# Optimization experiments

Measured on AMD Instinct MI355X. Metric: run time of the kernel, lower is better.

Reference implementation:

```python
import jax, jax.numpy as jnp
import numpy as np

B, N, D, H = 16, 576, 1024, 16
HD = D // H


def make_rel_indices(num_patches):
    # ConViT rel_indices: [N, N, 3] = (dx, dy, dx^2+dy^2) on a sqrt(N) grid
    img = int(num_patches ** 0.5)
    coords = np.arange(img)
    ind = coords.reshape(1, -1) - coords.reshape(-1, 1)  # [img, img]
    indx = np.tile(ind, (img, img))                      # repeats within rows
    indy = np.repeat(np.repeat(ind, img, axis=0), img, axis=1)
    indd = indx ** 2 + indy ** 2
    rel = np.stack([indx, indy, indd], axis=-1).astype(np.float32)  # [N, N, 3]
    return jnp.asarray(rel)


def setup_inputs() -> dict:
    key = jax.random.key(0)
    ks = jax.random.split(key, 8)
    s = D ** -0.5
    return {
        "x": jax.random.normal(ks[0], (B, N, D), jnp.float32),
        "W_qk": jax.random.normal(ks[1], (D, 2 * D), jnp.float32) * s,
        "W_v": jax.random.normal(ks[2], (D, D), jnp.float32) * s,
        "W_proj": jax.random.normal(ks[3], (D, D), jnp.float32) * s,
        "b_proj": jnp.zeros((D,), jnp.float32),
        "W_pos": jax.random.normal(ks[4], (3, H), jnp.float32) * 0.5,
        "b_pos": jnp.zeros((H,), jnp.float32),
        "gating": jnp.ones((H,), jnp.float32),
        "rel_indices": make_rel_indices(N),
    }


def reference(x, W_qk, W_v, W_proj, b_proj, W_pos, b_pos, gating, rel_indices):
    scale = HD ** -0.5
    qk = x @ W_qk                                  # [B, N, 2D]
    q = qk[..., :D].reshape(B, N, H, HD).transpose(0, 2, 1, 3)  # [B,H,N,HD]
    k = qk[..., D:].reshape(B, N, H, HD).transpose(0, 2, 1, 3)
    # content attention
    patch_score = jax.nn.softmax(jnp.einsum('bhnd,bhmd->bhnm', q, k) * scale, axis=-1)
    # learned positional attention from relative coordinates
    pos_logits = rel_indices @ W_pos + b_pos       # [N, N, H]
    pos_score = jax.nn.softmax(jnp.transpose(pos_logits, (2, 0, 1))[None], axis=-1)  # [1,H,N,N]
    # per-head gating mix, renormalized
    g = jax.nn.sigmoid(gating)[None, :, None, None]
    attn = (1.0 - g) * patch_score + g * pos_score
    attn = attn / attn.sum(axis=-1, keepdims=True)
    v = (x @ W_v).reshape(B, N, H, HD).transpose(0, 2, 1, 3)    # [B,H,N,HD]
    out = jnp.einsum('bhnm,bhmd->bhnd', attn, v)
    out = out.transpose(0, 2, 1, 3).reshape(B, N, D)
    return out @ W_proj + b_proj
```

## Files before the change

kernel.cpp:

```cpp
#include <hip/hip_runtime.h>
#include <hip/hip_bf16.h>
#include <math.h>

#define B_ 16
#define N_ 576
#define D_ 1024
#define H_ 16
#define HD_ 64
#define BN_ (B_ * N_)
#define LOG2E 1.4426950408889634f

typedef __bf16 bf16x8 __attribute__((ext_vector_type(8)));
typedef __bf16 bf16x4 __attribute__((ext_vector_type(4)));
typedef float  f32x4  __attribute__((ext_vector_type(4)));
typedef unsigned int u32x4 __attribute__((ext_vector_type(4)));

__device__ __forceinline__ unsigned pack_bf16x2(float a, float b)
{
    __bf16 lo = (__bf16)a, hi = (__bf16)b;
    unsigned short ul = __builtin_bit_cast(unsigned short, lo);
    unsigned short uh = __builtin_bit_cast(unsigned short, hi);
    return (unsigned)ul | ((unsigned)uh << 16);
}

__global__ __launch_bounds__(256) void prep(
    const float* __restrict__ x, const float* __restrict__ W_qk,
    const float* __restrict__ W_v, const float* __restrict__ W_proj,
    const float* __restrict__ W_pos, const float* __restrict__ gating,
    __bf16* __restrict__ xb, __bf16* __restrict__ wqkvt,
    __bf16* __restrict__ wpt, __bf16* __restrict__ Pp)
{
    __shared__ float t[64][65];
    const int bid = blockIdx.x;
    const int tid = threadIdx.x;

    if (bid < 9216) {
        size_t i = ((size_t)bid * 256 + tid) * 4;
        float4 v = *(const float4*)&x[i];
        bf16x4 o;
        o.x = (__bf16)v.x; o.y = (__bf16)v.y; o.z = (__bf16)v.z; o.w = (__bf16)v.w;
        *(bf16x4*)&xb[i] = o;
    } else if (bid < 10240) {
        int idx = bid - 9216;
        const float* W; __bf16* Wt; int N, bx, by;
        if (idx < 512)      { W = W_qk;   Wt = wqkvt;                          N = 2 * D_; bx = idx & 31; by = idx >> 5; }
        else if (idx < 768) { idx -= 512; W = W_v;    Wt = wqkvt + (size_t)2 * D_ * D_; N = D_; bx = idx & 15; by = idx >> 4; }
        else                { idx -= 768; W = W_proj; Wt = wpt;                N = D_;     bx = idx & 15; by = idx >> 4; }
        const int k0 = by * 64, n0 = bx * 64;
        const int r = tid >> 4, c4 = (tid & 15) << 2;
#pragma unroll
        for (int s = 0; s < 4; ++s) {
            int rr = r + (s << 4);
            float4 w = *(const float4*)&W[(size_t)(k0 + rr) * N + n0 + c4];
            t[rr][c4] = w.x; t[rr][c4 + 1] = w.y; t[rr][c4 + 2] = w.z; t[rr][c4 + 3] = w.w;
        }
        __syncthreads();
#pragma unroll
        for (int s = 0; s < 4; ++s) {
            int rr = r + (s << 4);
            bf16x4 o;
            o.x = (__bf16)t[c4 + 0][rr]; o.y = (__bf16)t[c4 + 1][rr];
            o.z = (__bf16)t[c4 + 2][rr]; o.w = (__bf16)t[c4 + 3][rr];
            *(bf16x4*)&Wt[(size_t)(n0 + rr) * D_ + k0 + c4] = o;
        }
    } else {
        int flat = (bid - 10240) * 4 + (tid >> 6);
        int h = flat / N_, n = flat % N_;
        int lane = tid & 63;
        const float w0 = W_pos[h] * LOG2E, w1 = W_pos[H_ + h] * LOG2E,
                    w2 = W_pos[2 * H_ + h] * LOG2E;
        const float rx = (float)(n % 24), ry = (float)(n / 24);
        float l2[9];
        float mx = -1e30f;
#pragma unroll
        for (int i = 0; i < 9; ++i) {
            int m = lane + (i << 6);
            float cx = (float)(m % 24), cy = (float)(m / 24);
            float dx = cx - rx, dy = cy - ry;
            float l = fmaf(w2, fmaf(dx, dx, dy * dy), fmaf(w0, dx, w1 * dy));
            l2[i] = l;
            mx = fmaxf(mx, l);
        }
#pragma unroll
        for (int off = 32; off; off >>= 1) mx = fmaxf(mx, __shfl_xor(mx, off, 64));
        float sum = 0.f;
#pragma unroll
        for (int i = 0; i < 9; ++i) sum += __builtin_amdgcn_exp2f(l2[i] - mx);
#pragma unroll
        for (int off = 32; off; off >>= 1) sum += __shfl_xor(sum, off, 64);
        float g = 1.f / (1.f + __expf(-gating[h]));
        float c = __log2f(g) - mx - __log2f(sum);
        __bf16* row = Pp + (size_t)(h * N_ + n) * N_;
#pragma unroll
        for (int i = 0; i < 9; ++i)
            row[(i << 6) + lane] = (__bf16)__builtin_amdgcn_exp2f(l2[i] + c);
    }
}

template<int OUTMODE>
__global__ __launch_bounds__(512, 2) void gemm256(
    const __bf16* __restrict__ A, const __bf16* __restrict__ Bt,
    const float* __restrict__ bias, void* __restrict__ Cp, void* __restrict__ Cp2,
    int M, int N, int nbn)
{
    __shared__ __bf16 As[2][256 * 64];
    __shared__ __bf16 Bs[2][256 * 64];

    const int tid = threadIdx.x;
    const int lane = tid & 63, wave = tid >> 6;
    const int fr = lane & 15, quad = lane >> 4;

    const int nwg = gridDim.x;
    const int wg = ((int)blockIdx.x & 7) * (nwg >> 3) + ((int)blockIdx.x >> 3);
    const int m0 = (wg / nbn) * 256;
    const int n0 = (wg % nbn) * 256;

    const int wm = (wave >> 2) * 128;
    const int wn = (wave & 3) * 64;

    int offA[2], offB[2], dA[2], dB[2];
#pragma unroll
    for (int r = 0; r < 2; ++r) {
        int rl = r * 64 + (tid >> 3);
        int pc = tid & 7;
        int l  = pc ^ (rl & 7);
        int rowA = (rl & 63) | ((rl & 64) << 1);
        int rowB = (rl & 31) + ((rl >> 5) << 6);
        offA[r] = (m0 + rowA) * 1024 + l * 8;
        offB[r] = (n0 + rowB) * 1024 + l * 8;
        int rlb = r * 64 + wave * 8;
        int rowAb = (rlb & 63) | ((rlb & 64) << 1);
        int rowBb = (rlb & 31) + ((rlb >> 5) << 6);
        dA[r] = rowAb * 64;
        dB[r] = rowBb * 64;
    }

    const int cA0 = (quad ^ (fr & 7)) * 8;
    const int cA1 = ((4 + quad) ^ (fr & 7)) * 8;

    f32x4 acc[8][4];
#pragma unroll
    for (int i = 0; i < 8; ++i)
#pragma unroll
        for (int j = 0; j < 4; ++j)
            acc[i][j] = (f32x4){0.f, 0.f, 0.f, 0.f};

    bf16x8 af[2][4];
    bf16x8 bfr[2][2][2];

#define GLL16(src, dst) __builtin_amdgcn_global_load_lds( \
    (const __attribute__((address_space(1))) void*)(src), \
    (__attribute__((address_space(3))) void*)(dst), 16, 0, 0)

#define ISSUE_A(U, BUF, KOFF) { \
    GLL16(A + offA[0] + (U) * 65536 + (KOFF), &As[BUF][dA[0] + (U) * 4096]); \
    GLL16(A + offA[1] + (U) * 65536 + (KOFF), &As[BUF][dA[1] + (U) * 4096]); }
#define ISSUE_B(U, BUF, KOFF) { \
    GLL16(Bt + offB[0] + (U) * 32768 + (KOFF), &Bs[BUF][dB[0] + (U) * 2048]); \
    GLL16(Bt + offB[1] + (U) * 32768 + (KOFF), &Bs[BUF][dB[1] + (U) * 2048]); }

#define READ_A(BUF, MH) { \
    const __bf16* _p = &As[BUF][(wm + (MH) * 64 + fr) * 64]; \
    _Pragma("unroll") for (int i = 0; i < 4; ++i) { \
        af[0][i] = *(const bf16x8*)&_p[i * 1024 + cA0]; \
        af[1][i] = *(const bf16x8*)&_p[i * 1024 + cA1]; } }

#define READ_B(BUF, NH) { \
    const __bf16* _p = &Bs[BUF][(wn + (NH) * 32 + fr) * 64]; \
    _Pragma("unroll") for (int j = 0; j < 2; ++j) { \
        bfr[NH][0][j] = *(const bf16x8*)&_p[j * 1024 + cA0]; \
        bfr[NH][1][j] = *(const bf16x8*)&_p[j * 1024 + cA1]; } }

#define MFMAQ(MH, NH) { \
    __builtin_amdgcn_s_setprio(1); \
    _Pragma("unroll") for (int i = 0; i < 4; ++i) \
    _Pragma("unroll") for (int j = 0; j < 2; ++j) { \
        f32x4 c = acc[(MH) * 4 + i][(NH) * 2 + j]; \
        c = __builtin_amdgcn_mfma_f32_16x16x32_bf16(af[0][i], bfr[NH][0][j], c, 0, 0, 0); \
        c = __builtin_amdgcn_mfma_f32_16x16x32_bf16(af[1][i], bfr[NH][1][j], c, 0, 0, 0); \
        acc[(MH) * 4 + i][(NH) * 2 + j] = c; } \
    __builtin_amdgcn_s_setprio(0); }

#define WAITV(N) asm volatile("s_waitcnt vmcnt(" #N ")" ::: "memory")
#define BARL() { asm volatile("s_waitcnt lgkmcnt(0)" ::: "memory"); \
                 asm volatile("s_barrier" ::: "memory"); }

#define ITER4(LAST) { \
   ISSUE_A(0, 1, kodd); ISSUE_B(0, 1, kodd); WAITV(6); BARL(); \
        READ_A(0, 0); READ_B(0, 0); READ_B(0, 1); MFMAQ(0, 0); MFMAQ(0, 1); \
   ISSUE_B(1, 1, kodd); ISSUE_A(1, 1, kodd); WAITV(8); BARL(); \
        READ_A(0, 1); MFMAQ(1, 0); MFMAQ(1, 1); \
   if (!(LAST)) { ISSUE_A(0, 0, keven); ISSUE_B(0, 0, keven); WAITV(6); } \
                       else { WAITV(2); } BARL(); \
        READ_A(1, 0); READ_B(1, 0); READ_B(1, 1); MFMAQ(0, 0); MFMAQ(0, 1); \
   if (!(LAST)) { ISSUE_B(1, 0, keven); ISSUE_A(1, 0, keven); WAITV(8); } \
                       else { WAITV(0); } BARL(); \
        READ_A(1, 1); MFMAQ(1, 0); MFMAQ(1, 1); }

    ISSUE_A(0, 0, 0); ISSUE_B(0, 0, 0); ISSUE_B(1, 0, 0); ISSUE_A(1, 0, 0);

#pragma unroll 1
    for (int it = 0; it < 7; ++it) {
        const int kodd  = it * 128 + 64;
        const int keven = it * 128 + 128;
        ITER4(0);
    }
    {
        const int kodd  = 7 * 128 + 64;
        const int keven = 0;
        ITER4(1);
    }

#undef ITER4
#undef WAITV
#undef BARL
#undef MFMAQ
#undef READ_B
#undef READ_A
#undef ISSUE_B
#undef ISSUE_A
#undef GLL16

    const int colb = n0 + wn + fr;
    const int rowb = m0 + wm + quad * 4;
#pragma unroll
    for (int j = 0; j < 4; ++j) {
        int col = colb + j * 16;
        float bv = (OUTMODE == 0 && bias) ? bias[col] : 0.0f;
#pragma unroll
        for (int i = 0; i < 8; ++i) {
            int row = rowb + i * 16;
            if (OUTMODE == 3) {
                if (col < 2048) {
#pragma unroll
                    for (int t = 0; t < 4; ++t)
                        ((__bf16*)Cp)[(size_t)(row + t) * 2048 + col] = (__bf16)acc[i][j][t];
                } else {
                    int bb = row / 576;
                    int ml = row - bb * 576;
                    bf16x4 o4;
#pragma unroll
                    for (int t = 0; t < 4; ++t) o4[t] = (__bf16)acc[i][j][t];
                    *(bf16x4*)&((__bf16*)Cp2)[((size_t)bb * 1024 + (col - 2048)) * 576 + ml] = o4;
                }
            } else {
#pragma unroll
                for (int t = 0; t < 4; ++t)
                    ((float*)Cp)[(size_t)(row + t) * N + col] = acc[i][j][t] + bv;
            }
        }
    }
}

__global__ __launch_bounds__(512, 2) void attn_mfma3(
    const __bf16* __restrict__ qk, const __bf16* __restrict__ vt,
    const __bf16* __restrict__ Pp, const float* __restrict__ gating,
    __bf16* __restrict__ ao)
{
    __shared__ __bf16 Ks[N_ * HD_];
    __shared__ __bf16 Vs[HD_ * N_];
    __shared__ __bf16 Sc[8 * 16 * 56];

    const int bid = blockIdx.x;
    const int h = bid & 15, b = bid >> 4;
    const int tid = threadIdx.x;
    const int lane = tid & 63, wave = tid >> 6;
    const int fr = lane & 15, quad = lane >> 4;

    const __bf16* qbase = qk + (size_t)b * N_ * (2 * D_) + h * HD_;
    const __bf16* kgl   = qbase + D_;
    const __bf16* vgl   = vt + (size_t)(b * H_ + h) * HD_ * N_;

#pragma unroll 3
    for (int it = 0; it < 9; ++it) {
        int s = it * 512 + tid;
        int r = s >> 3, p = s & 7;
        int l = p ^ (r & 7);
        __builtin_amdgcn_global_load_lds(
            (const __attribute__((address_space(1))) void*)(kgl + (size_t)r * (2 * D_) + l * 8),
            (__attribute__((address_space(3))) void*)&Ks[(size_t)(it * 512 + wave * 64) * 8],
            16, 0, 0);
        int d = s / 72, pv = s - d * 72;
        int lv = (pv & ~7) | ((pv & 7) ^ (d & 7));
        __builtin_amdgcn_global_load_lds(
            (const __attribute__((address_space(1))) void*)(vgl + (size_t)d * N_ + lv * 8),
            (__attribute__((address_space(3))) void*)&Vs[(size_t)(it * 512 + wave * 64) * 8],
            16, 0, 0);
    }
    __syncthreads();

    const float g   = 1.f / (1.f + __expf(-gating[h]));
    const float omg = 1.f - g;
    const float kk = 0.125f * LOG2E;

    __bf16* sw = &Sc[wave * 16 * 56];

    const int l0 = fr + 32 * (quad & 1);
    const int l1 = l0 + 16;
    const bool sel = (quad >> 1) != 0;

    for (int tt = wave; tt < 36; tt += 8) {
        const int n0 = tt * 16;

        const __bf16* qp = qbase + (size_t)(n0 + fr) * (2 * D_) + quad * 8;
        bf16x8 qf0 = *(const bf16x8*)qp;
        bf16x8 qf1 = *(const bf16x8*)(qp + 32);

        const __bf16* pprow = Pp + ((size_t)h * N_ + n0 + fr) * N_ + quad * 8;

        f32x4 S[36];
#pragma unroll
        for (int ct = 0; ct < 36; ++ct) {
            int row = ct * 16 + fr;
            int p0 = quad ^ (row & 7);
            int p1 = (4 + quad) ^ (row & 7);
            bf16x8 k0 = *(const bf16x8*)&Ks[row * 64 + p0 * 8];
            bf16x8 k1 = *(const bf16x8*)&Ks[row * 64 + p1 * 8];
            f32x4 a = (f32x4){0.f, 0.f, 0.f, 0.f};
            a = __builtin_amdgcn_mfma_f32_16x16x32_bf16(k0, qf0, a, 0, 0, 0);
            a = __builtin_amdgcn_mfma_f32_16x16x32_bf16(k1, qf1, a, 0, 0, 0);
            S[ct] = a;
        }

        float m01 = -1e30f, m23 = -1e30f;
#pragma unroll
        for (int ct = 0; ct < 36; ++ct) {
            m01 = fmaxf(m01, fmaxf(S[ct][0], S[ct][1]));
            m23 = fmaxf(m23, fmaxf(S[ct][2], S[ct][3]));
        }
        float m = fmaxf(m01, m23);
        m = fmaxf(m, __shfl_xor(m, 16, 64));
        m = fmaxf(m, __shfl_xor(m, 32, 64));
        float km = kk * m;
        float s0 = 0.f, s1 = 0.f, s2 = 0.f, s3 = 0.f;
#pragma unroll
        for (int ct = 0; ct < 36; ++ct) {
            float e0 = __builtin_amdgcn_exp2f(fmaf(kk, S[ct][0], -km));
            float e1 = __builtin_amdgcn_exp2f(fmaf(kk, S[ct][1], -km));
            float e2 = __builtin_amdgcn_exp2f(fmaf(kk, S[ct][2], -km));
            float e3 = __builtin_amdgcn_exp2f(fmaf(kk, S[ct][3], -km));
            S[ct][0] = e0; S[ct][1] = e1; S[ct][2] = e2; S[ct][3] = e3;
            s0 += e0; s1 += e1; s2 += e2; s3 += e3;
        }
        float s = (s0 + s1) + (s2 + s3);
        s += __shfl_xor(s, 16, 64);
        s += __shfl_xor(s, 32, 64);
        const float inv = omg / s;

        unsigned pk[72];
#pragma unroll
        for (int ct = 0; ct < 36; ++ct) {
            pk[2 * ct + 0] = pack_bf16x2(S[ct][0] * inv, S[ct][1] * inv);
            pk[2 * ct + 1] = pack_bf16x2(S[ct][2] * inv, S[ct][3] * inv);
        }

        f32x4 O[4];
#pragma unroll
        for (int dt = 0; dt < 4; ++dt) O[dt] = (f32x4){0.f, 0.f, 0.f, 0.f};

        bf16x8 posf = *(const bf16x8*)pprow;
#pragma unroll
        for (int kb = 0; kb < 18; ++kb) {
            bf16x8 posf_nxt = posf;
            if (kb < 17) posf_nxt = *(const bf16x8*)(pprow + (kb + 1) * 32);
            unsigned a0 = __shfl(pk[4 * kb + 0], l0, 64);
            unsigned a1 = __shfl(pk[4 * kb + 1], l0, 64);
            unsigned a2 = __shfl(pk[4 * kb + 2], l0, 64);
            unsigned a3 = __shfl(pk[4 * kb + 3], l0, 64);
            unsigned b0 = __shfl(pk[4 * kb + 0], l1, 64);
            unsigned b1 = __shfl(pk[4 * kb + 1], l1, 64);
            unsigned b2 = __shfl(pk[4 * kb + 2], l1, 64);
            unsigned b3 = __shfl(pk[4 * kb + 3], l1, 64);
            u32x4 w;
            w[0] = sel ? a2 : a0;
            w[1] = sel ? a3 : a1;
            w[2] = sel ? b2 : b0;
            w[3] = sel ? b3 : b1;
            bf16x8 pf = __builtin_bit_cast(bf16x8, w);
#pragma unroll
            for (int dt = 0; dt < 4; ++dt) {
                int d = dt * 16 + fr;
                int l = kb * 4 + quad;
                int p = (l & ~7) | ((l & 7) ^ (d & 7));
                bf16x8 vf = *(const bf16x8*)&Vs[d * 576 + p * 8];
                O[dt] = __builtin_amdgcn_mfma_f32_16x16x32_bf16(vf, pf,   O[dt], 0, 0, 0);
                O[dt] = __builtin_amdgcn_mfma_f32_16x16x32_bf16(vf, posf, O[dt], 0, 0, 0);
            }
            posf = posf_nxt;
        }

#pragma unroll
        for (int ps = 0; ps < 2; ++ps) {
#pragma unroll
            for (int dh = 0; dh < 2; ++dh) {
                int dt = 2 * ps + dh;
                bf16x4 o4;
#pragma unroll
                for (int t = 0; t < 4; ++t) o4[t] = (__bf16)O[dt][t];
                *(bf16x4*)&sw[fr * 56 + dh * 16 + quad * 4] = o4;
            }
            asm volatile("s_waitcnt lgkmcnt(0)" ::: "memory");
            {
                int row = lane >> 2;
                int off = (lane & 3) * 8;
                bf16x8 ov = *(const bf16x8*)&sw[row * 56 + off];
                *(bf16x8*)&ao[((size_t)b * N_ + n0 + row) * D_ + h * HD_ + ps * 32 + off] = ov;
            }
            asm volatile("s_waitcnt lgkmcnt(0)" ::: "memory");
        }
    }
}

extern "C" void kernel_launch(void* const* d_in, const int* in_sizes, int n_in,
                              void* d_out, int out_size, void* d_ws, size_t ws_size,
                              hipStream_t stream)
{
    const float* x      = (const float*)d_in[0];
    const float* W_qk   = (const float*)d_in[1];
    const float* W_v    = (const float*)d_in[2];
    const float* W_proj = (const float*)d_in[3];
    const float* b_proj = (const float*)d_in[4];
    const float* W_pos  = (const float*)d_in[5];
    const float* b_pos  = (const float*)d_in[6];
    const float* gating = (const float*)d_in[7];
    const float* rel    = (const float*)d_in[8];
    (void)b_pos; (void)rel;
    float* out = (float*)d_out;

    char* p = (char*)d_ws;
    __bf16* xb    = (__bf16*)p;  p += (size_t)BN_ * D_ * 2;
    __bf16* wqkvt = (__bf16*)p;  p += (size_t)(3 * D_) * D_ * 2;
    __bf16* wpt   = (__bf16*)p;  p += (size_t)D_ * D_ * 2;
    __bf16* qkb   = (__bf16*)p;  p += (size_t)BN_ * (2 * D_) * 2;
    __bf16* vt    = (__bf16*)p;  p += (size_t)BN_ * D_ * 2;
    __bf16* aob   = (__bf16*)p;  p += (size_t)BN_ * D_ * 2;
    __bf16* Pp    = (__bf16*)p;

    prep<<<12544, 256, 0, stream>>>(x, W_qk, W_v, W_proj, W_pos, gating,
                                    xb, wqkvt, wpt, Pp);
    gemm256<3><<<dim3((BN_ / 256) * (3 * D_ / 256)), 512, 0, stream>>>(
        xb, wqkvt, nullptr, qkb, vt, BN_, 3 * D_, 3 * D_ / 256);
    attn_mfma3<<<B_ * H_, 512, 0, stream>>>(qkb, vt, Pp, gating, aob);
    gemm256<0><<<dim3((BN_ / 256) * (D_ / 256)), 512, 0, stream>>>(
        aob, wpt, b_proj, out, nullptr, BN_, D_, D_ / 256);
}
```

Baseline: 274.3 us.

## Split attention across two blocks per head, read V from global, stage V-transpose stores

The attention kernel now launches two blocks per (batch, head), each handling half the query tiles, and drops the shared-memory copy of V in favour of direct global reads, which shrinks LDS use and should raise occupancy and parallelism. Attention output is written head-major ([H,B,N,64]) directly from registers, and the projection GEMM's A-operand addressing is changed to match that layout. The QKV GEMM's transposed V write path now stages tiles through shared memory so global stores are coalesced 16-byte writes. The trade-off is redundant K loading per half-block and uncached global V reads inside the inner MFMA loop.

Measured after the change: 635.7 us. +131.8%, slower.

```diff
diff --git a/kernel.cpp b/kernel.cpp
--- a/kernel.cpp
+++ b/kernel.cpp
@@ -103,8 +103,7 @@
     const float* __restrict__ bias, void* __restrict__ Cp, void* __restrict__ Cp2,
     int M, int N, int nbn)
 {
-    __shared__ __bf16 As[2][256 * 64];
-    __shared__ __bf16 Bs[2][256 * 64];
+    __shared__ __bf16 SMEM[67584];
 
     const int tid = threadIdx.x;
     const int lane = tid & 63, wave = tid >> 6;
@@ -126,7 +125,8 @@
         int l  = pc ^ (rl & 7);
         int rowA = (rl & 63) | ((rl & 64) << 1);
         int rowB = (rl & 31) + ((rl >> 5) << 6);
-        offA[r] = (m0 + rowA) * 1024 + l * 8;
+        offA[r] = (OUTMODE == 0) ? ((m0 + rowA) * 64 + l * 8)
+                                 : ((m0 + rowA) * 1024 + l * 8);
         offB[r] = (n0 + rowB) * 1024 + l * 8;
         int rlb = r * 64 + wave * 8;
         int rowAb = (rlb & 63) | ((rlb & 64) << 1);
@@ -152,21 +152,23 @@
     (const __attribute__((address_space(1))) void*)(src), \
     (__attribute__((address_space(3))) void*)(dst), 16, 0, 0)
 
+#define AOFF(U, KOFF) (OUTMODE == 0 ? ((U) * 4096 + (KOFF) * 9216) \
+                                    : ((U) * 65536 + (KOFF)))
 #define ISSUE_A(U, BUF, KOFF) { \
-    GLL16(A + offA[0] + (U) * 65536 + (KOFF), &As[BUF][dA[0] + (U) * 4096]); \
-    GLL16(A + offA[1] + (U) * 65536 + (KOFF), &As[BUF][dA[1] + (U) * 4096]); }
+    GLL16(A + offA[0] + AOFF(U, KOFF), &SMEM[(BUF) * 16384 + dA[0] + (U) * 4096]); \
+    GLL16(A + offA[1] + AOFF(U, KOFF), &SMEM[(BUF) * 16384 + dA[1] + (U) * 4096]); }
 #define ISSUE_B(U, BUF, KOFF) { \
-    GLL16(Bt + offB[0] + (U) * 32768 + (KOFF), &Bs[BUF][dB[0] + (U) * 2048]); \
-    GLL16(Bt + offB[1] + (U) * 32768 + (KOFF), &Bs[BUF][dB[1] + (U) * 2048]); }
+    GLL16(Bt + offB[0] + (U) * 32768 + (KOFF), &SMEM[32768 + (BUF) * 16384 + dB[0] + (U) * 2048]); \
+    GLL16(Bt + offB[1] + (U) * 32768 + (KOFF), &SMEM[32768 + (BUF) * 16384 + dB[1] + (U) * 2048]); }
 
 #define READ_A(BUF, MH) { \
-    const __bf16* _p = &As[BUF][(wm + (MH) * 64 + fr) * 64]; \
+    const __bf16* _p = &SMEM[(BUF) * 16384 + (wm + (MH) * 64 + fr) * 64]; \
     _Pragma("unroll") for (int i = 0; i < 4; ++i) { \
         af[0][i] = *(const bf16x8*)&_p[i * 1024 + cA0]; \
         af[1][i] = *(const bf16x8*)&_p[i * 1024 + cA1]; } }
 
 #define READ_B(BUF, NH) { \
-    const __bf16* _p = &Bs[BUF][(wn + (NH) * 32 + fr) * 64]; \
+    const __bf16* _p = &SMEM[32768 + (BUF) * 16384 + (wn + (NH) * 32 + fr) * 64]; \
     _Pragma("unroll") for (int j = 0; j < 2; ++j) { \
         bfr[NH][0][j] = *(const bf16x8*)&_p[j * 1024 + cA0]; \
         bfr[NH][1][j] = *(const bf16x8*)&_p[j * 1024 + cA1]; } }
@@ -219,34 +221,55 @@
 #undef READ_A
 #undef ISSUE_B
 #undef ISSUE_A
+#undef AOFF
 #undef GLL16
 
-    const int colb = n0 + wn + fr;
-    const int rowb = m0 + wm + quad * 4;
-#pragma unroll
-    for (int j = 0; j < 4; ++j) {
-        int col = colb + j * 16;
-        float bv = (OUTMODE == 0 && bias) ? bias[col] : 0.0f;
-#pragma unroll
-        for (int i = 0; i < 8; ++i) {
-            int row = rowb + i * 16;
-            if (OUTMODE == 3) {
-                if (col < 2048) {
+    if (OUTMODE == 3 && n0 >= 2048) {
+        asm volatile("s_waitcnt lgkmcnt(0)" ::: "memory");
+        __syncthreads();
+#pragma unroll
+        for (int j = 0; j < 4; ++j) {
+            int dl = wn + fr + j * 16;
+#pragma unroll
+            for (int i = 0; i < 8; ++i) {
+                int mb = wm + quad * 4 + i * 16;
+                bf16x4 o4;
+#pragma unroll
+                for (int t = 0; t < 4; ++t) o4[t] = (__bf16)acc[i][j][t];
+                *(bf16x4*)&SMEM[dl * 264 + mb] = o4;
+            }
+        }
+        __syncthreads();
+        const int dcol = n0 - 2048;
+#pragma unroll
+        for (int it2 = 0; it2 < 16; ++it2) {
+            int f = it2 * 512 + tid;
+            int d = f >> 5, mseg = (f & 31) << 3;
+            int gm = m0 + mseg;
+            int bb = gm / 576;
+            int ml = gm - bb * 576;
+            bf16x8 v = *(const bf16x8*)&SMEM[d * 264 + mseg];
+            *(bf16x8*)&((__bf16*)Cp2)[((size_t)bb * 1024 + dcol + d) * 576 + ml] = v;
+        }
+    } else {
+        const int colb = n0 + wn + fr;
+        const int rowb = m0 + wm + quad * 4;
+#pragma unroll
+        for (int j = 0; j < 4; ++j) {
+            int col = colb + j * 16;
+            float bv = (OUTMODE == 0 && bias) ? bias[col] : 0.0f;
+#pragma unroll
+            for (int i = 0; i < 8; ++i) {
+                int row = rowb + i * 16;
+                if (OUTMODE == 3) {
 #pragma unroll
                     for (int t = 0; t < 4; ++t)
                         ((__bf16*)Cp)[(size_t)(row + t) * 2048 + col] = (__bf16)acc[i][j][t];
                 } else {
-                    int bb = row / 576;
-                    int ml = row - bb * 576;
-                    bf16x4 o4;
-#pragma unroll
-                    for (int t = 0; t < 4; ++t) o4[t] = (__bf16)acc[i][j][t];
-                    *(bf16x4*)&((__bf16*)Cp2)[((size_t)bb * 1024 + (col - 2048)) * 576 + ml] = o4;
+#pragma unroll
+                    for (int t = 0; t < 4; ++t)
+                        ((float*)Cp)[(size_t)(row + t) * N + col] = acc[i][j][t] + bv;
                 }
-            } else {
-#pragma unroll
-                for (int t = 0; t < 4; ++t)
-                    ((float*)Cp)[(size_t)(row + t) * N + col] = acc[i][j][t] + bv;
             }
         }
     }
@@ -258,11 +281,11 @@
     __bf16* __restrict__ ao)
 {
     __shared__ __bf16 Ks[N_ * HD_];
-    __shared__ __bf16 Vs[HD_ * N_];
-    __shared__ __bf16 Sc[8 * 16 * 56];
 
     const int bid = blockIdx.x;
-    const int h = bid & 15, b = bid >> 4;
+    const int half = bid & 1;
+    const int hb = bid >> 1;
+    const int h = hb & 15, b = hb >> 4;
     const int tid = threadIdx.x;
     const int lane = tid & 63, wave = tid >> 6;
     const int fr = lane & 15, quad = lane >> 4;
@@ -280,12 +303,6 @@
             (const __attribute__((address_space(1))) void*)(kgl + (size_t)r * (2 * D_) + l * 8),
             (__attribute__((address_space(3))) void*)&Ks[(size_t)(it * 512 + wave * 64) * 8],
             16, 0, 0);
-        int d = s / 72, pv = s - d * 72;
-        int lv = (pv & ~7) | ((pv & 7) ^ (d & 7));
-        __builtin_amdgcn_global_load_lds(
-            (const __attribute__((address_space(1))) void*)(vgl + (size_t)d * N_ + lv * 8),
-            (__attribute__((address_space(3))) void*)&Vs[(size_t)(it * 512 + wave * 64) * 8],
-            16, 0, 0);
     }
     __syncthreads();
 
@@ -293,14 +310,12 @@
     const float omg = 1.f - g;
     const float kk = 0.125f * LOG2E;
 
-    __bf16* sw = &Sc[wave * 16 * 56];
-
     const int l0 = fr + 32 * (quad & 1);
     const int l1 = l0 + 16;
     const bool sel = (quad >> 1) != 0;
 
-    for (int tt = wave; tt < 36; tt += 8) {
-        const int n0 = tt * 16;
+    for (int tt2 = wave; tt2 < 18; tt2 += 8) {
+        const int n0 = (half * 18 + tt2) * 16;
 
         const __bf16* qp = qbase + (size_t)(n0 + fr) * (2 * D_) + quad * 8;
         bf16x8 qf0 = *(const bf16x8*)qp;
@@ -357,6 +372,8 @@
         f32x4 O[4];
 #pragma unroll
         for (int dt = 0; dt < 4; ++dt) O[dt] = (f32x4){0.f, 0.f, 0.f, 0.f};
+
+        const __bf16* vbase = vgl + (size_t)fr * N_ + quad * 8;
 
         bf16x8 posf = *(const bf16x8*)pprow;
 #pragma unroll
@@ -379,34 +396,22 @@
             bf16x8 pf = __builtin_bit_cast(bf16x8, w);
 #pragma unroll
             for (int dt = 0; dt < 4; ++dt) {
-                int d = dt * 16 + fr;
-                int l = kb * 4 + quad;
-                int p = (l & ~7) | ((l & 7) ^ (d & 7));
-                bf16x8 vf = *(const bf16x8*)&Vs[d * 576 + p * 8];
+                bf16x8 vf = *(const bf16x8*)(vbase + (size_t)dt * 16 * N_ + kb * 32);
                 O[dt] = __builtin_amdgcn_mfma_f32_16x16x32_bf16(vf, pf,   O[dt], 0, 0, 0);
                 O[dt] = __builtin_amdgcn_mfma_f32_16x16x32_bf16(vf, posf, O[dt], 0, 0, 0);
             }
             posf = posf_nxt;
         }
 
-#pragma unroll
-        for (int ps = 0; ps < 2; ++ps) {
-#pragma unroll
-            for (int dh = 0; dh < 2; ++dh) {
-                int dt = 2 * ps + dh;
+        {
+            __bf16* aorow = ao + ((size_t)(h * B_ + b) * N_ + n0 + fr) * 64 + quad * 4;
+#pragma unroll
+            for (int dt = 0; dt < 4; ++dt) {
                 bf16x4 o4;
 #pragma unroll
                 for (int t = 0; t < 4; ++t) o4[t] = (__bf16)O[dt][t];
-                *(bf16x4*)&sw[fr * 56 + dh * 16 + quad * 4] = o4;
+                *(bf16x4*)(aorow + dt * 16) = o4;
             }
-            asm volatile("s_waitcnt lgkmcnt(0)" ::: "memory");
-            {
-                int row = lane >> 2;
-                int off = (lane & 3) * 8;
-                bf16x8 ov = *(const bf16x8*)&sw[row * 56 + off];
-                *(bf16x8*)&ao[((size_t)b * N_ + n0 + row) * D_ + h * HD_ + ps * 32 + off] = ov;
-            }
-            asm volatile("s_waitcnt lgkmcnt(0)" ::: "memory");
         }
     }
 }
@@ -440,7 +445,7 @@
                                     xb, wqkvt, wpt, Pp);
     gemm256<3><<<dim3((BN_ / 256) * (3 * D_ / 256)), 512, 0, stream>>>(
         xb, wqkvt, nullptr, qkb, vt, BN_, 3 * D_, 3 * D_ / 256);
-    attn_mfma3<<<B_ * H_, 512, 0, stream>>>(qkb, vt, Pp, gating, aob);
+    attn_mfma3<<<2 * B_ * H_, 512, 0, stream>>>(qkb, vt, Pp, gating, aob);
     gemm256<0><<<dim3((BN_ / 256) * (D_ / 256)), 512, 0, stream>>>(
         aob, wpt, b_proj, out, nullptr, BN_, D_, D_ / 256);
 }
```
